# Kernel tuning notes

Measured on AMD Instinct MI355X. Metric: run time of the kernel, lower is better.

## Reference

```python
import jax, jax.numpy as jnp
import numpy as np

# ---- model hyperparameters (from init_kwargs) ----
PATTERN_SPECS = ((6, 50), (5, 50), (4, 50), (3, 50))  # (pattern_len, num_patterns)
MAX_LEN = max(pl for pl, _ in PATTERN_SPECS)          # 6
P = sum(n for _, n in PATTERN_SPECS)                  # 200 total patterns
LM1 = MAX_LEN - 1                                     # 5 transitions per pattern
EMB_DIM = 300
N_LOCAL = 10000
BIAS_SCALE = 1.0
TAU = 0.0
LN_EPS = 1e-5
NEG_INF = -jnp.inf
# end state (index into hidden dim of size MAX_LEN) per pattern
END_STATES = jnp.asarray([pl - 1 for pl, n in PATTERN_SPECS for _ in range(n)], dtype=jnp.int32)  # [P]


def setup_inputs() -> dict:
    key = jax.random.key(0)
    ks = jax.random.split(key, 8)
    B, T = 128, 256
    local_embeddings = jax.random.normal(ks[0], (EMB_DIM, N_LOCAL), jnp.float32)
    diags = jax.random.normal(ks[1], (P * LM1, EMB_DIM), jnp.float32) * 0.05   # xavier-ish
    bias = jax.random.normal(ks[2], (P * LM1, 1), jnp.float32) * 0.05
    wildcards = jax.random.normal(ks[3], (P, LM1), jnp.float32) * 0.05
    linear_w = jax.random.normal(ks[4], (2, P), jnp.float32) * 0.05
    linear_b = jax.random.normal(ks[5], (2,), jnp.float32) * 0.05
    docs = jax.random.randint(ks[6], (B, T), 0, N_LOCAL, dtype=jnp.int32)
    doc_lens = jax.random.randint(ks[7], (B,), MAX_LEN - 1, T + 1, dtype=jnp.int32)
    return {"local_embeddings": local_embeddings, "diags": diags, "bias": bias,
            "wildcards": wildcards, "linear_w": linear_w, "linear_b": linear_b,
            "docs": docs, "doc_lens": doc_lens}


def reference(local_embeddings, diags, bias, wildcards, linear_w, linear_b, docs, doc_lens):
    # Max-sum semiring: times=add, plus=max, one=0, zero=-inf, outer maps = identity.
    B, T = docs.shape
    # transition scores for every local-vocab token: [N_LOCAL, P*LM1]
    trans = (jnp.matmul(diags, local_embeddings) + BIAS_SCALE * bias).T
    tm = trans[docs].reshape(B, T, P, LM1)            # [B,T,P,LM1]
    wc = wildcards                                     # wildcard_scale = one = 0 under max-sum
    restart = jnp.zeros((B, P, 1), trans.dtype)        # semiring.one
    hid0 = jnp.concatenate([jnp.zeros((B, P, 1), trans.dtype),
                            jnp.full((B, P, LM1), NEG_INF, trans.dtype)], axis=2)  # [B,P,MAX_LEN]
    scores0 = jnp.full((B, P), NEG_INF, trans.dtype)
    active = (jnp.arange(T)[None, :] < doc_lens[:, None]).T  # [T,B]

    def step(carry, xt):
        hid, sc = carry
        tm_t, m_t = xt                                 # [B,P,LM1], [B]
        prev = hid[:, :, :-1]
        new = jnp.maximum(prev + tm_t, prev + wc[None])   # main vs wildcard transition
        hid = jnp.concatenate([restart, new], axis=2)
        endv = jnp.take_along_axis(hid, END_STATES[None, :, None].astype(jnp.int32), axis=2)[..., 0]  # [B,P]
        sc = jnp.where(m_t[:, None], jnp.maximum(sc, endv), sc)
        return (hid, sc), None

    (_, scores), _ = jax.lax.scan(step, (hid0, scores0), (jnp.transpose(tm, (1, 0, 2, 3)), active))

    # replace never-completed patterns (-inf) with the per-row min of finite scores
    neg_mask = scores == NEG_INF
    s = jnp.where(neg_mask, jnp.inf, scores)
    row_min = jnp.min(s, axis=1, keepdims=True)
    s = jnp.where(jnp.isinf(s), row_min, s)
    # LayerNorm without affine
    mu = jnp.mean(s, axis=-1, keepdims=True)
    var = jnp.var(s, axis=-1, keepdims=True)
    s = (s - mu) / jnp.sqrt(var + LN_EPS)
    # STE binarizer forward
    s = (s > TAU).astype(trans.dtype)
    # final linear
    return jnp.matmul(s, linear_w.T) + linear_b
```

## Files before the change

### kernel.cpp

```cpp
#include <hip/hip_runtime.h>
#include <math.h>

#define EMB   300
#define NLOC  10000
#define PP    200
#define NN    1000
#define BB    128
#define TT    256
#define NSEG  8
#define SEGLEN 32

#define NVBLK 79
#define NNBLK 8
#define NKPAN 40
#define LOSCALE 4096.f

typedef _Float16 f16x8 __attribute__((ext_vector_type(8)));
typedef float    f32x4 __attribute__((ext_vector_type(4)));

__global__ __launch_bounds__(128) void split_a(const float* __restrict__ emb,
                                               _Float16* __restrict__ Ah,
                                               _Float16* __restrict__ Al) {
    const int m    = threadIdx.x;
    const int vblk = blockIdx.x;
    const int kpan = blockIdx.y;
    const int v    = vblk * 128 + m;
    const size_t outb = ((size_t)(vblk * NKPAN + kpan) * 128 + m) * 8;
    _Float16 hi[8], lo[8];
    #pragma unroll
    for (int j = 0; j < 8; ++j) {
        int e = kpan * 8 + j;
        float x = (v < NLOC && e < EMB) ? emb[(size_t)e * NLOC + v] : 0.f;
        _Float16 h = (_Float16)x;
        float r = (x - (float)h) * LOSCALE;
        hi[j] = h;
        lo[j] = (_Float16)r;
    }
    *(f16x8*)&Ah[outb] = *(const f16x8*)hi;
    *(f16x8*)&Al[outb] = *(const f16x8*)lo;
}

__global__ __launch_bounds__(128) void split_b(const float* __restrict__ diags,
                                               _Float16* __restrict__ Bh,
                                               _Float16* __restrict__ Bl) {
    const int nn   = threadIdx.x;
    const int nblk = blockIdx.x;
    const int kpan = blockIdx.y;
    const int n    = nblk * 128 + nn;
    const size_t outb = ((size_t)(nblk * NKPAN + kpan) * 128 + nn) * 8;
    _Float16 hi[8], lo[8];
    #pragma unroll
    for (int j = 0; j < 8; ++j) {
        int e = kpan * 8 + j;
        float x = (n < NN && e < EMB) ? diags[(size_t)n * EMB + e] : 0.f;
        _Float16 h = (_Float16)x;
        float r = (x - (float)h) * LOSCALE;
        hi[j] = h;
        lo[j] = (_Float16)r;
    }
    *(f16x8*)&Bh[outb] = *(const f16x8*)hi;
    *(f16x8*)&Bl[outb] = *(const f16x8*)lo;
}

__global__ __launch_bounds__(256, 2) void gemm_reg(
    const _Float16* __restrict__ Ah, const _Float16* __restrict__ Al,
    const _Float16* __restrict__ Bh, const _Float16* __restrict__ Bl,
    const float* __restrict__ bias, float* __restrict__ trans, int tstr) {
    const int tid  = threadIdx.x;
    const int vblk = blockIdx.x;
    const int nblk = blockIdx.y;

    const int lane = tid & 63;
    const int wave = tid >> 6;
    const int wr   = wave >> 1;
    const int wc   = wave & 1;
    const int l15  = lane & 15;
    const int hh   = lane >> 4;

    const size_t aoff = (size_t)vblk * (NKPAN * 1024) + (size_t)hh * 1024 + (size_t)(wr * 64 + l15) * 8;
    const size_t boff = (size_t)nblk * (NKPAN * 1024) + (size_t)hh * 1024 + (size_t)(wc * 64 + l15) * 8;
    const _Float16* pAh = Ah + aoff;
    const _Float16* pAl = Al + aoff;
    const _Float16* pBh = Bh + boff;
    const _Float16* pBl = Bl + boff;

    f32x4 acc_h[4][4] = {};
    f32x4 acc_m[4][4] = {};

    #pragma unroll
    for (int s = 0; s < 10; ++s) {
        f16x8 fah[4], fal[4], fbh[4], fbl[4];
        #pragma unroll
        for (int i = 0; i < 4; ++i) {
            fah[i] = *(const f16x8*)(pAh + s * 4096 + i * 128);
            fal[i] = *(const f16x8*)(pAl + s * 4096 + i * 128);
            fbh[i] = *(const f16x8*)(pBh + s * 4096 + i * 128);
            fbl[i] = *(const f16x8*)(pBl + s * 4096 + i * 128);
        }
        #pragma unroll
        for (int i = 0; i < 4; ++i)
            #pragma unroll
            for (int j = 0; j < 4; ++j) {
                acc_h[i][j] = __builtin_amdgcn_mfma_f32_16x16x32_f16(fah[i], fbh[j], acc_h[i][j], 0, 0, 0);
                acc_m[i][j] = __builtin_amdgcn_mfma_f32_16x16x32_f16(fah[i], fbl[j], acc_m[i][j], 0, 0, 0);
                acc_m[i][j] = __builtin_amdgcn_mfma_f32_16x16x32_f16(fal[i], fbh[j], acc_m[i][j], 0, 0, 0);
            }
    }

    __shared__ float etile[64][132];

    #pragma unroll 1
    for (int h = 0; h < 2; ++h) {
        __syncthreads();
        if (wr == h) {
            #pragma unroll
            for (int i = 0; i < 4; ++i)
                #pragma unroll
                for (int j = 0; j < 4; ++j)
                    #pragma unroll
                    for (int r = 0; r < 4; ++r)
                        etile[i * 16 + hh * 4 + r][wc * 64 + j * 16 + l15] =
                            acc_h[i][j][r] + acc_m[i][j][r] * (1.f / LOSCALE);
        }
        __syncthreads();
        #pragma unroll
        for (int it = 0; it < 8; ++it) {
            const int idx = it * 256 + tid;
            const int row = idx >> 5;
            const int c4  = (idx & 31) * 4;
            const int v   = vblk * 128 + h * 64 + row;
            const int n   = nblk * 128 + c4;
            if (v < NLOC && n + 3 < NN) {
                float4 val = *(const float4*)&etile[row][c4];
                const float4 b4 = *(const float4*)&bias[n];
                val.x += b4.x; val.y += b4.y; val.z += b4.z; val.w += b4.w;
                *(float4*)&trans[(size_t)v * tstr + n] = val;
            }
        }
    }
}

__global__ __launch_bounds__(256) void trans_gemm(const float* __restrict__ emb,
                                                  const float* __restrict__ diags,
                                                  const float* __restrict__ bias,
                                                  float* __restrict__ trans) {
    const int tid = threadIdx.x;
    const int tn  = tid & 15;
    const int tv  = tid >> 4;
    const int v0  = blockIdx.x * 128;
    const int n0  = blockIdx.y * 128;
    __shared__ float As[15][132];
    __shared__ float Bs[15][132];
    float acc[8][8] = {};
    for (int kk = 0; kk < 20; ++kk) {
        const int e0 = kk * 15;
        #pragma unroll
        for (int l = tid; l < 480; l += 256) {
            int k = l >> 5, c = l & 31;
            int v = v0 + c * 4;
            const float* src = emb + (size_t)(e0 + k) * NLOC + v;
            float4 val;
            if (v + 3 < NLOC) val = *(const float4*)src;
            else {
                val.x = (v + 0 < NLOC) ? src[0] : 0.f;
                val.y = (v + 1 < NLOC) ? src[1] : 0.f;
                val.z = (v + 2 < NLOC) ? src[2] : 0.f;
                val.w = (v + 3 < NLOC) ? src[3] : 0.f;
            }
            *(float4*)&As[k][c * 4] = val;
        }
        for (int l = tid; l < 1920; l += 256) {
            int nn = l / 15, k = l - nn * 15;
            int n = n0 + nn;
            Bs[k][nn] = (n < NN) ? diags[n * EMB + e0 + k] : 0.f;
        }
        __syncthreads();
        #pragma unroll
        for (int k = 0; k < 15; ++k) {
            float4 a0 = *(const float4*)&As[k][tv * 4];
            float4 a1 = *(const float4*)&As[k][tv * 4 + 64];
            float4 b0 = *(const float4*)&Bs[k][tn * 4];
            float4 b1 = *(const float4*)&Bs[k][tn * 4 + 64];
            float av[8] = {a0.x, a0.y, a0.z, a0.w, a1.x, a1.y, a1.z, a1.w};
            float bv[8] = {b0.x, b0.y, b0.z, b0.w, b1.x, b1.y, b1.z, b1.w};
            #pragma unroll
            for (int i = 0; i < 8; ++i)
                #pragma unroll
                for (int j = 0; j < 8; ++j)
                    acc[i][j] += av[i] * bv[j];
        }
        __syncthreads();
    }
    #pragma unroll
    for (int i = 0; i < 8; ++i) {
        int v = v0 + (i >> 2) * 64 + tv * 4 + (i & 3);
        if (v >= NLOC) continue;
        #pragma unroll
        for (int jh = 0; jh < 2; ++jh) {
            int n = n0 + jh * 64 + tn * 4;
            if (n + 3 < NN) {
                float4 r;
                r.x = acc[i][jh * 4 + 0] + bias[n + 0];
                r.y = acc[i][jh * 4 + 1] + bias[n + 1];
                r.z = acc[i][jh * 4 + 2] + bias[n + 2];
                r.w = acc[i][jh * 4 + 3] + bias[n + 3];
                *(float4*)&trans[(size_t)v * NN + n] = r;
            } else {
                #pragma unroll
                for (int j = 0; j < 4; ++j)
                    if (n + j < NN)
                        trans[(size_t)v * NN + n + j] = acc[i][jh * 4 + j] + bias[n + j];
            }
        }
    }
}

__global__ __launch_bounds__(256) void scan_seg(const float* __restrict__ trans,
                                                const float* __restrict__ wildcards,
                                                const int* __restrict__ docs,
                                                const int* __restrict__ doc_lens,
                                                float* __restrict__ partial, int tstr) {
    const int b   = blockIdx.x;
    const int seg = blockIdx.y;
    const int tid = threadIdx.x;
    __shared__ int sdoc[TT];
    sdoc[tid] = docs[b * TT + tid];
    __syncthreads();

    const bool act = tid < PP;
    const int  p   = act ? tid : (PP - 1);
    const int  p5  = p * 5;
    const int  len = doc_lens[b];
    const int  t0  = seg * SEGLEN;
    const int  start = (t0 - 4 > 0) ? t0 - 4 : 0;
    const int  end   = (t0 + SEGLEN < len) ? t0 + SEGLEN : len;

    const float NI = -INFINITY;
    float score = NI;

    if (start < end) {
        const float w0 = wildcards[p5 + 0];
        const float w1 = wildcards[p5 + 1];
        const float w2 = wildcards[p5 + 2];
        const float w3 = wildcards[p5 + 3];
        const float w4 = wildcards[p5 + 4];
        const int e = (p < 50) ? 5 : (p < 100) ? 4 : (p < 150) ? 3 : 2;

        float h1 = NI, h2 = NI, h3 = NI, h4 = NI, h5 = NI;
        const int nt   = end - start;
        const int ntm1 = nt - 1;

        float A[5], B[5], C[5];
#define LOADR(R, idx) { int tt = (idx); tt = (tt < ntm1) ? tt : ntm1;          \
        const float* r_ = trans + (size_t)sdoc[start + tt] * tstr + p5;        \
        R[0] = r_[0]; R[1] = r_[1]; R[2] = r_[2]; R[3] = r_[3]; R[4] = r_[4]; }
#define STEP(R, t) { \
        float u0 = fmaxf(R[0], w0), u1 = fmaxf(R[1], w1), u2 = fmaxf(R[2], w2);\
        float u3 = fmaxf(R[3], w3), u4 = fmaxf(R[4], w4);                      \
        h5 = h4 + u4; h4 = h3 + u3; h3 = h2 + u2; h2 = h1 + u1; h1 = u0;       \
        if ((t) >= t0) {                                                       \
            float endv = (e == 5) ? h5 : (e == 4) ? h4 : (e == 3) ? h3 : h2;   \
            score = fmaxf(score, endv);                                        \
        } }

        LOADR(A, 0); LOADR(B, 1); LOADR(C, 2);
        for (int i = 0; i < nt; i += 3) {
            STEP(A, start + i);
            LOADR(A, i + 3);
            if (i + 1 < nt) { STEP(B, start + i + 1); }
            LOADR(B, i + 4);
            if (i + 2 < nt) { STEP(C, start + i + 2); }
            LOADR(C, i + 5);
        }
#undef LOADR
#undef STEP
    }

    if (act) partial[((size_t)b * NSEG + seg) * PP + p] = score;
}

__device__ inline float block_sum_bcast(float v, volatile float* red, int tid) {
    #pragma unroll
    for (int o = 32; o > 0; o >>= 1) v += __shfl_down(v, o, 64);
    __syncthreads();
    if ((tid & 63) == 0) red[tid >> 6] = v;
    __syncthreads();
    return red[0] + red[1] + red[2] + red[3];
}

__global__ __launch_bounds__(256) void finalize(const float* __restrict__ partial,
                                                const float* __restrict__ linear_w,
                                                const float* __restrict__ linear_b,
                                                float* __restrict__ out) {
    const int b   = blockIdx.x;
    const int tid = threadIdx.x;
    __shared__ float red[4];

    const bool act = tid < PP;
    const int  p   = act ? tid : (PP - 1);

    float m = -INFINITY;
    #pragma unroll
    for (int s = 0; s < NSEG; ++s)
        m = fmaxf(m, partial[((size_t)b * NSEG + s) * PP + p]);

    float total = block_sum_bcast(act ? m : 0.f, red, tid);
    float mu = total * (1.f / (float)PP);

    int bin = (act && m > mu) ? 1 : 0;
    float c0 = bin ? linear_w[p]      : 0.f;
    float c1 = bin ? linear_w[PP + p] : 0.f;

    float r0 = block_sum_bcast(c0, red, tid);
    float r1 = block_sum_bcast(c1, red, tid);

    if (tid == 0) {
        out[b * 2 + 0] = r0 + linear_b[0];
        out[b * 2 + 1] = r1 + linear_b[1];
    }
}

extern "C" void kernel_launch(void* const* d_in, const int* in_sizes, int n_in,
                              void* d_out, int out_size, void* d_ws, size_t ws_size,
                              hipStream_t stream) {
    const float* emb    = (const float*)d_in[0];
    const float* diags  = (const float*)d_in[1];
    const float* bias   = (const float*)d_in[2];
    const float* wc     = (const float*)d_in[3];
    const float* lw     = (const float*)d_in[4];
    const float* lb     = (const float*)d_in[5];
    const int*   docs   = (const int*)d_in[6];
    const int*   dlens  = (const int*)d_in[7];
    float*       out    = (float*)d_out;

    const size_t aElems = (size_t)NVBLK * NKPAN * 128 * 8;
    const size_t bElems = (size_t)NNBLK * NKPAN * 128 * 8;
    const size_t partialElems = (size_t)BB * NSEG * PP;
    const size_t f16Bytes = (2 * aElems + 2 * bElems) * sizeof(_Float16);

    int tstr;
    {
        const size_t need1024 = ((size_t)NLOC * 1024 + partialElems) * 4 + f16Bytes;
        const size_t need1000 = ((size_t)NLOC * 1000 + partialElems) * 4 + f16Bytes;
        if (ws_size >= need1024)       tstr = 1024;
        else if (ws_size >= need1000)  tstr = 1000;
        else                           tstr = 0;
    }

    float* trans   = (float*)d_ws;
    float* partial = trans + (size_t)NLOC * (tstr ? tstr : 1000);
    _Float16* Ah = (_Float16*)(partial + partialElems);
    _Float16* Al = Ah + aElems;
    _Float16* Bh = Al + aElems;
    _Float16* Bl = Bh + bElems;

    if (tstr) {
        split_a<<<dim3(NVBLK, NKPAN, 1), 128, 0, stream>>>(emb, Ah, Al);
        split_b<<<dim3(NNBLK, NKPAN, 1), 128, 0, stream>>>(diags, Bh, Bl);
        gemm_reg<<<dim3(NVBLK, NNBLK, 1), 256, 0, stream>>>(Ah, Al, Bh, Bl, bias, trans, tstr);
        scan_seg<<<dim3(BB, NSEG, 1), 256, 0, stream>>>(trans, wc, docs, dlens, partial, tstr);
    } else {
        trans_gemm<<<dim3(79, 8, 1), 256, 0, stream>>>(emb, diags, bias, trans);
        scan_seg<<<dim3(BB, NSEG, 1), 256, 0, stream>>>(trans, wc, docs, dlens, partial, 1000);
    }
    finalize<<<BB, 256, 0, stream>>>(partial, lw, lb, out);
}
```

Measured before the change: 68.69 us.

## Split GEMM into single-wave 64x64 blocks with swizzled block order

Replaces the 256-thread, 4-wave GEMM block (128x128 tile) with 64-thread blocks that each compute a 64x64 tile, launched as a 1D grid of 2528 blocks. A swizzle on the block index groups neighbouring tiles for cache locality. Bias is added in registers before the shared-memory staging, and the two-pass shared epilogue is replaced by one pass. This gives more, smaller blocks to fill the CUs and removes the cross-wave syncs, at the cost of losing reuse of A/B fragments shared between waves in the same block. Stores now also fill the padding columns up to tstr, where the old code stopped at the real output width.

Result: no change. 69.89 us (+1.7%).

```diff
diff --git a/kernel.cpp b/kernel.cpp
--- a/kernel.cpp
+++ b/kernel.cpp
@@ -62,23 +62,25 @@
     *(f16x8*)&Bl[outb] = *(const f16x8*)lo;
 }
 
-__global__ __launch_bounds__(256, 2) void gemm_reg(
+__global__ __launch_bounds__(64) void gemm_w64(
     const _Float16* __restrict__ Ah, const _Float16* __restrict__ Al,
     const _Float16* __restrict__ Bh, const _Float16* __restrict__ Bl,
     const float* __restrict__ bias, float* __restrict__ trans, int tstr) {
-    const int tid  = threadIdx.x;
-    const int vblk = blockIdx.x;
-    const int nblk = blockIdx.y;
-
-    const int lane = tid & 63;
-    const int wave = tid >> 6;
-    const int wr   = wave >> 1;
-    const int wc   = wave & 1;
+    __shared__ float etile[64][68];
+
+    const int lane = threadIdx.x;
     const int l15  = lane & 15;
     const int hh   = lane >> 4;
 
-    const size_t aoff = (size_t)vblk * (NKPAN * 1024) + (size_t)hh * 1024 + (size_t)(wr * 64 + l15) * 8;
-    const size_t boff = (size_t)nblk * (NKPAN * 1024) + (size_t)hh * 1024 + (size_t)(wc * 64 + l15) * 8;
+    const int bid   = blockIdx.x;
+    const int swz   = (bid & 7) * 316 + (bid >> 3);
+    const int vblk2 = swz >> 4;
+    const int nblk2 = swz & 15;
+    const int vblk  = vblk2 >> 1, mhalf = (vblk2 & 1) * 64;
+    const int nblk  = nblk2 >> 1, nhalf = (nblk2 & 1) * 64;
+
+    const size_t aoff = (size_t)vblk * (NKPAN * 1024) + (size_t)hh * 1024 + (size_t)(mhalf + l15) * 8;
+    const size_t boff = (size_t)nblk * (NKPAN * 1024) + (size_t)hh * 1024 + (size_t)(nhalf + l15) * 8;
     const _Float16* pAh = Ah + aoff;
     const _Float16* pAl = Al + aoff;
     const _Float16* pBh = Bh + boff;
@@ -107,36 +109,32 @@
             }
     }
 
-    __shared__ float etile[64][132];
-
-    #pragma unroll 1
-    for (int h = 0; h < 2; ++h) {
-        __syncthreads();
-        if (wr == h) {
+    float bj[4];
+    #pragma unroll
+    for (int j = 0; j < 4; ++j) {
+        const int n = nblk2 * 64 + j * 16 + l15;
+        bj[j] = (n < NN) ? bias[n] : 0.f;
+    }
+
+    #pragma unroll
+    for (int i = 0; i < 4; ++i)
+        #pragma unroll
+        for (int j = 0; j < 4; ++j)
             #pragma unroll
-            for (int i = 0; i < 4; ++i)
-                #pragma unroll
-                for (int j = 0; j < 4; ++j)
-                    #pragma unroll
-                    for (int r = 0; r < 4; ++r)
-                        etile[i * 16 + hh * 4 + r][wc * 64 + j * 16 + l15] =
-                            acc_h[i][j][r] + acc_m[i][j][r] * (1.f / LOSCALE);
-        }
-        __syncthreads();
-        #pragma unroll
-        for (int it = 0; it < 8; ++it) {
-            const int idx = it * 256 + tid;
-            const int row = idx >> 5;
-            const int c4  = (idx & 31) * 4;
-            const int v   = vblk * 128 + h * 64 + row;
-            const int n   = nblk * 128 + c4;
-            if (v < NLOC && n + 3 < NN) {
-                float4 val = *(const float4*)&etile[row][c4];
-                const float4 b4 = *(const float4*)&bias[n];
-                val.x += b4.x; val.y += b4.y; val.z += b4.z; val.w += b4.w;
-                *(float4*)&trans[(size_t)v * tstr + n] = val;
-            }
-        }
+            for (int r = 0; r < 4; ++r)
+                etile[i * 16 + hh * 4 + r][j * 16 + l15] =
+                    acc_h[i][j][r] + acc_m[i][j][r] * (1.f / LOSCALE) + bj[j];
+    __syncthreads();
+
+    #pragma unroll
+    for (int it = 0; it < 16; ++it) {
+        const int idx = it * 64 + lane;
+        const int row = idx >> 4;
+        const int c4  = (idx & 15) * 4;
+        const int v   = vblk2 * 64 + row;
+        const int n   = nblk2 * 64 + c4;
+        if (v < NLOC && n + 3 < tstr)
+            *(float4*)&trans[(size_t)v * tstr + n] = *(const float4*)&etile[row][c4];
     }
 }
 
@@ -357,7 +355,7 @@
     if (tstr) {
         split_a<<<dim3(NVBLK, NKPAN, 1), 128, 0, stream>>>(emb, Ah, Al);
         split_b<<<dim3(NNBLK, NKPAN, 1), 128, 0, stream>>>(diags, Bh, Bl);
-        gemm_reg<<<dim3(NVBLK, NNBLK, 1), 256, 0, stream>>>(Ah, Al, Bh, Bl, bias, trans, tstr);
+        gemm_w64<<<dim3(158 * 16, 1, 1), 64, 0, stream>>>(Ah, Al, Bh, Bl, bias, trans, tstr);
         scan_seg<<<dim3(BB, NSEG, 1), 256, 0, stream>>>(trans, wc, docs, dlens, partial, tstr);
     } else {
         trans_gemm<<<dim3(79, 8, 1), 256, 0, stream>>>(emb, diags, bias, trans);
```
